# Kernel tuning notes

Hardware: AMD Instinct MI355X
Metric: run time of the kernel (lower is better)

Reference implementation:

```python
import jax, jax.numpy as jnp
import numpy as np

N_NODES = 50000
N_EDGES = 800000
IN_FEATS = 128
H_FEATS = 128
NUM_CLASSES = 64


def _linear_params(key, fan_in, fan_out):
    kw, kb = jax.random.split(key)
    bound = 1.0 / np.sqrt(fan_in)
    W = jax.random.uniform(kw, (fan_out, fan_in), minval=-bound, maxval=bound, dtype=jnp.float32)
    b = jax.random.uniform(kb, (fan_out,), minval=-bound, maxval=bound, dtype=jnp.float32)
    return W, b


def setup_inputs() -> dict:
    key = jax.random.key(0)
    k_feat, k_src, k_dst, k1, k2, k3 = jax.random.split(key, 6)
    in_feat = jax.random.normal(k_feat, (N_NODES, IN_FEATS), dtype=jnp.float32)
    src = jax.random.randint(k_src, (N_EDGES,), 0, N_NODES, dtype=jnp.int32)
    dst = jax.random.randint(k_dst, (N_EDGES,), 0, N_NODES, dtype=jnp.int32)
    W1, b1 = _linear_params(k1, IN_FEATS, H_FEATS)
    W2, b2 = _linear_params(k2, H_FEATS, H_FEATS)
    W3, b3 = _linear_params(k3, H_FEATS, NUM_CLASSES)
    return {"in_feat": in_feat, "W1": W1, "b1": b1, "W2": W2, "b2": b2,
            "W3": W3, "b3": b3, "src": src, "dst": dst}


def reference(in_feat, W1, b1, W2, b2, W3, b3, src, dst):
    N = in_feat.shape[0]

    def gin_layer(x, W, b):
        # DGL GINConv with eps=0: (x + sum of in-neighbor messages) -> Linear
        agg = jax.ops.segment_sum(x[src], dst, num_segments=N)  # [N, d]
        return jax.nn.relu((x + agg) @ W.T + b)

    h = gin_layer(in_feat, W1, b1)
    h = gin_layer(h, W2, b2)
    h = gin_layer(h, W3, b3)
    return h
```

## Files before the change

### kernel.cpp

```cpp
#include <hip/hip_runtime.h>

typedef _Float16 half8 __attribute__((ext_vector_type(8)));
typedef float floatx4 __attribute__((ext_vector_type(4)));
typedef unsigned int uintx4 __attribute__((ext_vector_type(4)));

union AB { uint4 u; half8 h; };
union H2 { unsigned int u; _Float16 h[2]; };
union US16 { uintx4 u[2]; unsigned short s[16]; };

#define CAPLOG 6
#define CAP 64

__global__ __launch_bounds__(256) void histA_init_k(
    const int* __restrict__ dst, int* __restrict__ histG, int E, int nbins,
    const float* __restrict__ F, const float* __restrict__ W1,
    const float* __restrict__ W2, const float* __restrict__ W3,
    _Float16* __restrict__ hX, _Float16* __restrict__ W1h,
    _Float16* __restrict__ W2h, _Float16* __restrict__ W3h,
    _Float16* __restrict__ hZ,
    int n4f, int n4w1, int n4w2, int n4w3, int zoffX4, int zoffZ4) {
    int t = threadIdx.x;
    if (blockIdx.x < 256) {
        __shared__ int h[256];
        h[t] = 0;
        __syncthreads();
        int per = (E + 255) / 256;
        int beg = blockIdx.x * per;
        int end = min(E, beg + per);
        for (int e = beg + t; e < end; e += 256)
            atomicAdd(&h[dst[e] >> 8], 1);
        __syncthreads();
        for (int i = t; i < nbins; i += 256)
            histG[i * 256 + blockIdx.x] = h[i];
        return;
    }
    int i = (blockIdx.x - 256) * 256 + t;
    const float* X;
    _Float16* O;
    int j;
    if (i < n4f) { X = F; O = hX; j = i; }
    else if (i < n4f + n4w1) { X = W1; O = W1h; j = i - n4f; }
    else if (i < n4f + n4w1 + n4w2) { X = W2; O = W2h; j = i - n4f - n4w1; }
    else if (i < n4f + n4w1 + n4w2 + n4w3) { X = W3; O = W3h; j = i - n4f - n4w1 - n4w2; }
    else {
        int z = i - (n4f + n4w1 + n4w2 + n4w3);
        if (z < 16) ((uint4*)hX)[zoffX4 + z] = make_uint4(0, 0, 0, 0);
        else if (z < 24) ((uint4*)hZ)[zoffZ4 + (z - 16)] = make_uint4(0, 0, 0, 0);
        return;
    }
    float4 v = reinterpret_cast<const float4*>(X)[j];
    union { uint2 u; _Float16 h[4]; } o;
    o.h[0] = (_Float16)v.x; o.h[1] = (_Float16)v.y;
    o.h[2] = (_Float16)v.z; o.h[3] = (_Float16)v.w;
    reinterpret_cast<uint2*>(O)[j] = o.u;
}

__global__ __launch_bounds__(1024) void scan1_k(const int* __restrict__ x,
                                                int* __restrict__ inc,
                                                int* __restrict__ partial, int n) {
    __shared__ int sd[1024];
    int t = threadIdx.x;
    int v = blockIdx.x * 1024 + t;
    sd[t] = (v < n) ? x[v] : 0;
    __syncthreads();
    for (int off = 1; off < 1024; off <<= 1) {
        int val = (t >= off) ? sd[t - off] : 0;
        __syncthreads();
        sd[t] += val;
        __syncthreads();
    }
    if (v < n) inc[v] = sd[t];
    if (t == 1023) partial[blockIdx.x] = sd[1023];
}

__global__ __launch_bounds__(256) void scatterB_k(const int* __restrict__ src,
                                                  const int* __restrict__ dst,
                                                  const int* __restrict__ inc,
                                                  const int* __restrict__ histG,
                                                  const int* __restrict__ partial, int nparts,
                                                  unsigned int* __restrict__ binned,
                                                  int E, int nbins) {
    __shared__ int cur[256];
    __shared__ int pp[64];
    int t = threadIdx.x, blk = blockIdx.x;
    if (t < 64) {
        int v = (t < nparts) ? partial[t] : 0;
        for (int off = 1; off < 64; off <<= 1) {
            int n = __shfl_up(v, off, 64);
            if (t >= off) v += n;
        }
        int ex = __shfl_up(v, 1, 64);
        if (t == 0) ex = 0;
        pp[t] = ex;
    }
    __syncthreads();
    for (int i = t; i < nbins; i += 256) {
        int idx = i * 256 + blk;
        cur[i] = inc[idx] + pp[idx >> 10] - histG[idx];
    }
    __syncthreads();
    int per = (E + 255) / 256;
    int beg = blk * per;
    int end = min(E, beg + per);
    for (int e = beg + t; e < end; e += 256) {
        int d = dst[e];
        int s = src[e];
        int pos = atomicAdd(&cur[d >> 8], 1);
        binned[pos] = ((unsigned int)(d & 255) << 16) | (unsigned int)s;
    }
}

__global__ __launch_bounds__(256) void binB_k(const unsigned int* __restrict__ binned,
                                              const int* __restrict__ inc,
                                              const int* __restrict__ histG,
                                              const int* __restrict__ partial, int nparts,
                                              unsigned short* __restrict__ col,
                                              int* __restrict__ cnt,
                                              int N, int E, int nbins) {
    __shared__ unsigned short lcol[256 * CAP];
    __shared__ int lcnt[256];
    __shared__ int pp[64];
    __shared__ int bounds[2];
    int t = threadIdx.x;
    int b = blockIdx.x;
    if (t < 64) {
        int v = (t < nparts) ? partial[t] : 0;
        for (int off = 1; off < 64; off <<= 1) {
            int n = __shfl_up(v, off, 64);
            if (t >= off) v += n;
        }
        int ex = __shfl_up(v, 1, 64);
        if (t == 0) ex = 0;
        pp[t] = ex;
    }
    unsigned int* lcol32 = (unsigned int*)lcol;
    for (int i = t; i < 256 * CAP / 2; i += 256) lcol32[i] = 0xFFFFFFFFu;
    lcnt[t] = 0;
    __syncthreads();
    if (t == 0) {
        int i0 = b * 256;
        bounds[0] = inc[i0] + pp[i0 >> 10] - histG[i0];
    } else if (t == 1) {
        if (b == nbins - 1) bounds[1] = E;
        else {
            int i1 = (b + 1) * 256;
            bounds[1] = inc[i1] + pp[i1 >> 10] - histG[i1];
        }
    }
    __syncthreads();
    int beg = bounds[0], end = bounds[1];
    for (int e = beg + t; e < end; e += 256) {
        unsigned int u = binned[e];
        int dl = u >> 16;
        int pos = atomicAdd(&lcnt[dl], 1);
        if (pos < CAP) lcol[(dl << CAPLOG) + pos] = (unsigned short)(u & 0xFFFFu);
    }
    __syncthreads();
    int base = b << 8;
    int nodes = min(256, N - base);
    uint4* colg = (uint4*)(col + ((size_t)base << CAPLOG));
    const uint4* coll = (const uint4*)lcol;
    for (int i = t; i < nodes * 8; i += 256) colg[i] = coll[i];
    for (int i = t; i < nodes; i += 256) cnt[base + i] = lcnt[i];
}

__global__ __launch_bounds__(256) void aggregate_k(const _Float16* __restrict__ X,
                                                   const int* __restrict__ cnt,
                                                   const unsigned short* __restrict__ col,
                                                   _Float16* __restrict__ Y,
                                                   int nnodes) {
    int b = blockIdx.x;
    int xcd = b & 7;
    int h = xcd >> 2;
    int ng = (b >> 3) * 4 + (xcd & 3);
    int lane = threadIdx.x & 63;
    int fl = lane & 31;
    int node = ng * 8 + (threadIdx.x >> 6) * 2 + (lane >> 5);
    if (node >= nnodes) return;
    const unsigned int* X32 = (const unsigned int*)X;
    int hoff = h << 5;

    int deg = cnt[node];
    if (deg > CAP) deg = CAP;
    int degp = (deg + 15) & ~15;
    const unsigned short* c = col + ((size_t)node << CAPLOG);

    float a[8], bb[8];
#pragma unroll
    for (int j = 0; j < 8; j++) { a[j] = 0.f; bb[j] = 0.f; }

    for (int e = 0; e < degp; e += 16) {
        US16 ix;
        ix.u[0] = *reinterpret_cast<const uintx4*>(c + e);
        ix.u[1] = *reinterpret_cast<const uintx4*>(c + e + 8);
        H2 u[16];
#pragma unroll
        for (int j = 0; j < 16; j++) {
            int s = (int)ix.s[j];
            s = (s < nnodes) ? s : nnodes;
            u[j].u = X32[(size_t)s * 64 + hoff + fl];
        }
#pragma unroll
        for (int j = 0; j < 8; j++) {
            a[j] += (float)u[j].h[0] + (float)u[j + 8].h[0];
            bb[j] += (float)u[j].h[1] + (float)u[j + 8].h[1];
        }
    }

    H2 xs, r;
    xs.u = X32[(size_t)node * 64 + hoff + fl];
    float s0 = ((a[0] + a[1]) + (a[2] + a[3])) + ((a[4] + a[5]) + (a[6] + a[7]));
    float s1 = ((bb[0] + bb[1]) + (bb[2] + bb[3])) + ((bb[4] + bb[5]) + (bb[6] + bb[7]));
    r.h[0] = (_Float16)((float)xs.h[0] + s0);
    r.h[1] = (_Float16)((float)xs.h[1] + s1);
    __builtin_nontemporal_store(r.u, reinterpret_cast<unsigned int*>(Y) + (size_t)node * 64 + hoff + fl);
}

__global__ __launch_bounds__(256) void agg_final_k(const _Float16* __restrict__ Z,
                                                   const int* __restrict__ cnt,
                                                   const unsigned short* __restrict__ col,
                                                   const float* __restrict__ bias,
                                                   float* __restrict__ out, int nnodes) {
    int lane = threadIdx.x & 63;
    int fl = lane & 31;
    int node = blockIdx.x * 8 + (threadIdx.x >> 6) * 2 + (lane >> 5);
    if (node >= nnodes) return;
    const unsigned int* Z32 = (const unsigned int*)Z;

    int deg = cnt[node];
    if (deg > CAP) deg = CAP;
    int degp = (deg + 15) & ~15;
    const unsigned short* c = col + ((size_t)node << CAPLOG);

    float a[8], bb[8];
#pragma unroll
    for (int j = 0; j < 8; j++) { a[j] = 0.f; bb[j] = 0.f; }

    for (int e = 0; e < degp; e += 16) {
        US16 ix;
        ix.u[0] = *reinterpret_cast<const uintx4*>(c + e);
        ix.u[1] = *reinterpret_cast<const uintx4*>(c + e + 8);
        H2 u[16];
#pragma unroll
        for (int j = 0; j < 16; j++) {
            int s = (int)ix.s[j];
            s = (s < nnodes) ? s : nnodes;
            u[j].u = Z32[(size_t)s * 32 + fl];
        }
#pragma unroll
        for (int j = 0; j < 8; j++) {
            a[j] += (float)u[j].h[0] + (float)u[j + 8].h[0];
            bb[j] += (float)u[j].h[1] + (float)u[j + 8].h[1];
        }
    }

    H2 xs;
    xs.u = Z32[(size_t)node * 32 + fl];
    float2 bv = reinterpret_cast<const float2*>(bias)[fl];
    float s0 = ((a[0] + a[1]) + (a[2] + a[3])) + ((a[4] + a[5]) + (a[6] + a[7]));
    float s1 = ((bb[0] + bb[1]) + (bb[2] + bb[3])) + ((bb[4] + bb[5]) + (bb[6] + bb[7]));
    float2 r;
    r.x = fmaxf((float)xs.h[0] + s0 + bv.x, 0.f);
    r.y = fmaxf((float)xs.h[1] + s1 + bv.y, 0.f);
    reinterpret_cast<float2*>(out)[(size_t)node * 32 + fl] = r;
}

template <int NOUT, bool RAW>
__global__ __launch_bounds__(256) void gemm_mfma_k(const _Float16* __restrict__ Y,
                                                   const _Float16* __restrict__ Wh,
                                                   const float* __restrict__ bias,
                                                   _Float16* __restrict__ out, int nnodes) {
    constexpr int NT = NOUT / 16;
    constexpr int WSTR = 136;
    __shared__ _Float16 Wl[NOUT * WSTR];
    __shared__ float Bl[NOUT];

    const int t = threadIdx.x;
    for (int p = t; p < NOUT * 16; p += 256) {
        int f = p >> 4;
        int kq = (p & 15) * 8;
        uint4 u = *reinterpret_cast<const uint4*>(Wh + f * 128 + kq);
        *reinterpret_cast<uint4*>(&Wl[f * WSTR + kq]) = u;
    }
    if (!RAW && t < NOUT) Bl[t] = bias[t];
    __syncthreads();

    const int wave = t >> 6;
    const int lane = t & 63;
    const int quad = lane >> 4;
    const int fcol = lane & 15;
    const int m_base = (blockIdx.x * 4 + wave) * 16;
    const int row = m_base + fcol;
    const bool rowok = row < nnodes;

    floatx4 acc[NT];
#pragma unroll
    for (int ft = 0; ft < NT; ft++) acc[ft] = (floatx4){0.f, 0.f, 0.f, 0.f};

    const uint4* Yrow = reinterpret_cast<const uint4*>(Y + (size_t)row * 128);
#pragma unroll
    for (int step = 0; step < 4; step++) {
        AB a;
        if (rowok) a.u = Yrow[step * 4 + quad];
        else       a.u = make_uint4(0u, 0u, 0u, 0u);
#pragma unroll
        for (int ft = 0; ft < NT; ft++) {
            half8 b = *reinterpret_cast<const half8*>(
                &Wl[(ft * 16 + fcol) * WSTR + step * 32 + quad * 8]);
            acc[ft] = __builtin_amdgcn_mfma_f32_16x16x32_f16(a.h, b, acc[ft], 0, 0, 0);
        }
    }

#pragma unroll
    for (int ft = 0; ft < NT; ft++) {
        int f = ft * 16 + fcol;
        float bv = RAW ? 0.f : Bl[f];
#pragma unroll
        for (int r = 0; r < 4; r++) {
            int node = m_base + quad * 4 + r;
            if (node < nnodes) {
                float v = acc[ft][r] + bv;
                if (!RAW) v = fmaxf(v, 0.f);
                out[(size_t)node * NOUT + f] = (_Float16)v;
            }
        }
    }
}

extern "C" void kernel_launch(void* const* d_in, const int* in_sizes, int n_in,
                              void* d_out, int out_size, void* d_ws, size_t ws_size,
                              hipStream_t stream) {
    const float* in_feat = (const float*)d_in[0];
    const float* W1 = (const float*)d_in[1];
    const float* b1 = (const float*)d_in[2];
    const float* W2 = (const float*)d_in[3];
    const float* b2 = (const float*)d_in[4];
    const float* W3 = (const float*)d_in[5];
    const float* b3 = (const float*)d_in[6];
    const int* src = (const int*)d_in[7];
    const int* dst = (const int*)d_in[8];
    float* out = (float*)d_out;

    const int N = in_sizes[0] / 128;
    const int E = in_sizes[7];
    const int szW1 = in_sizes[1];
    const int szW2 = in_sizes[3];
    const int szW3 = in_sizes[5];
    const int nbins = (N + 255) >> 8;
    const int nhist = nbins * 256;

    char* p = (char*)d_ws;
    int* cnt = (int*)p;               p += (size_t)N * 4;
    unsigned short* col = (unsigned short*)p; p += (size_t)N * CAP * 2;
    int* histG = (int*)p;             p += (size_t)nhist * 4;
    int* incS = (int*)p;              p += (size_t)nhist * 4;
    int* partial = (int*)p;           p += 256;
    unsigned int* binned = (unsigned int*)p; p += (size_t)E * 4;
    _Float16* hX = (_Float16*)p;      p += (size_t)(N + 1) * 128 * 2;
    _Float16* hB = (_Float16*)p;      p += (size_t)N * 128 * 2;
    _Float16* hZ = (_Float16*)p;      p += (size_t)(N + 1) * 64 * 2;
    _Float16* W1h = (_Float16*)p;     p += (size_t)szW1 * 2;
    _Float16* W2h = (_Float16*)p;     p += (size_t)szW2 * 2;
    _Float16* W3h = (_Float16*)p;     p += (size_t)szW3 * 2;

    const int nblk_scan = (nhist + 1023) / 1024;

    {
        int n4f = N * 128 / 4;
        int total = n4f + szW1 / 4 + szW2 / 4 + szW3 / 4 + 32;
        int iblk = (total + 255) / 256;
        histA_init_k<<<256 + iblk, 256, 0, stream>>>(dst, histG, E, nbins,
                                                     in_feat, W1, W2, W3,
                                                     hX, W1h, W2h, W3h, hZ,
                                                     n4f, szW1 / 4, szW2 / 4, szW3 / 4,
                                                     N * 16, N * 8);
    }
    scan1_k<<<nblk_scan, 1024, 0, stream>>>(histG, incS, partial, nhist);
    scatterB_k<<<256, 256, 0, stream>>>(src, dst, incS, histG, partial, nblk_scan,
                                        binned, E, nbins);
    binB_k<<<nbins, 256, 0, stream>>>(binned, incS, histG, partial, nblk_scan,
                                      col, cnt, N, E, nbins);

    const int ngrp8 = (N + 7) / 8;
    const int nblk_agg = ((ngrp8 + 3) / 4) * 8;
    const int nblk_gemm = (N + 63) / 64;
    aggregate_k<<<nblk_agg, 256, 0, stream>>>(hX, cnt, col, hB, N);
    gemm_mfma_k<128, false><<<nblk_gemm, 256, 0, stream>>>(hB, W1h, b1, hX, N);
    aggregate_k<<<nblk_agg, 256, 0, stream>>>(hX, cnt, col, hB, N);
    gemm_mfma_k<128, false><<<nblk_gemm, 256, 0, stream>>>(hB, W2h, b2, hX, N);
    gemm_mfma_k<64, true><<<nblk_gemm, 256, 0, stream>>>(hX, W3h, nullptr, hZ, N);
    agg_final_k<<<(N + 7) / 8, 256, 0, stream>>>(hZ, cnt, col, b3, out, N);
}
```

Measured before the change: 264.3 us.

## Use packed fp16 accumulation and one wave per node in aggregation

The aggregation kernels now accumulate neighbor features with packed half2 adds into 16 fp16 partial accumulators, converting to fp32 only for the final reduction, instead of converting every value to float. The main aggregate kernel also drops the XCD-aware split of feature halves across blocks and assigns one full 64-lane wave per node covering all 128 features. This cuts conversion and ALU work and simplifies indexing, but fp16 partial sums lose precision and the L2 locality of the previous XCD mapping is given up.

New measurement: 238.7 us. -9.7%, faster.

```diff
diff --git a/kernel.cpp b/kernel.cpp
--- a/kernel.cpp
+++ b/kernel.cpp
@@ -1,11 +1,13 @@
 #include <hip/hip_runtime.h>
 
 typedef _Float16 half8 __attribute__((ext_vector_type(8)));
+typedef _Float16 half2v __attribute__((ext_vector_type(2)));
 typedef float floatx4 __attribute__((ext_vector_type(4)));
 typedef unsigned int uintx4 __attribute__((ext_vector_type(4)));
 
 union AB { uint4 u; half8 h; };
 union H2 { unsigned int u; _Float16 h[2]; };
+union H2P { unsigned int u; half2v h; };
 union US16 { uintx4 u[2]; unsigned short s[16]; };
 
 #define CAPLOG 6
@@ -169,51 +171,45 @@
                                                    const unsigned short* __restrict__ col,
                                                    _Float16* __restrict__ Y,
                                                    int nnodes) {
-    int b = blockIdx.x;
-    int xcd = b & 7;
-    int h = xcd >> 2;
-    int ng = (b >> 3) * 4 + (xcd & 3);
+    int w = blockIdx.x * 4 + (threadIdx.x >> 6);
     int lane = threadIdx.x & 63;
-    int fl = lane & 31;
-    int node = ng * 8 + (threadIdx.x >> 6) * 2 + (lane >> 5);
-    if (node >= nnodes) return;
-    const unsigned int* X32 = (const unsigned int*)X;
-    int hoff = h << 5;
-
-    int deg = cnt[node];
+    if (w >= nnodes) return;
+    const unsigned int* X32 = reinterpret_cast<const unsigned int*>(X);
+    int deg = cnt[w];
     if (deg > CAP) deg = CAP;
     int degp = (deg + 15) & ~15;
-    const unsigned short* c = col + ((size_t)node << CAPLOG);
-
-    float a[8], bb[8];
-#pragma unroll
-    for (int j = 0; j < 8; j++) { a[j] = 0.f; bb[j] = 0.f; }
+    const unsigned short* c = col + ((size_t)w << CAPLOG);
+
+    H2P acc[16];
+#pragma unroll
+    for (int j = 0; j < 16; j++) acc[j].u = 0u;
 
     for (int e = 0; e < degp; e += 16) {
         US16 ix;
         ix.u[0] = *reinterpret_cast<const uintx4*>(c + e);
         ix.u[1] = *reinterpret_cast<const uintx4*>(c + e + 8);
-        H2 u[16];
+        H2P u[16];
 #pragma unroll
         for (int j = 0; j < 16; j++) {
             int s = (int)ix.s[j];
             s = (s < nnodes) ? s : nnodes;
-            u[j].u = X32[(size_t)s * 64 + hoff + fl];
-        }
-#pragma unroll
-        for (int j = 0; j < 8; j++) {
-            a[j] += (float)u[j].h[0] + (float)u[j + 8].h[0];
-            bb[j] += (float)u[j].h[1] + (float)u[j + 8].h[1];
-        }
-    }
-
+            u[j].u = X32[(size_t)s * 64 + lane];
+        }
+#pragma unroll
+        for (int j = 0; j < 16; j++) acc[j].h += u[j].h;
+    }
+
+    float s0 = 0.f, s1 = 0.f;
+#pragma unroll
+    for (int j = 0; j < 16; j++) {
+        s0 += (float)acc[j].h[0];
+        s1 += (float)acc[j].h[1];
+    }
     H2 xs, r;
-    xs.u = X32[(size_t)node * 64 + hoff + fl];
-    float s0 = ((a[0] + a[1]) + (a[2] + a[3])) + ((a[4] + a[5]) + (a[6] + a[7]));
-    float s1 = ((bb[0] + bb[1]) + (bb[2] + bb[3])) + ((bb[4] + bb[5]) + (bb[6] + bb[7]));
+    xs.u = X32[(size_t)w * 64 + lane];
     r.h[0] = (_Float16)((float)xs.h[0] + s0);
     r.h[1] = (_Float16)((float)xs.h[1] + s1);
-    __builtin_nontemporal_store(r.u, reinterpret_cast<unsigned int*>(Y) + (size_t)node * 64 + hoff + fl);
+    __builtin_nontemporal_store(r.u, reinterpret_cast<unsigned int*>(Y) + (size_t)w * 64 + lane);
 }
 
 __global__ __launch_bounds__(256) void agg_final_k(const _Float16* __restrict__ Z,
@@ -232,15 +228,15 @@
     int degp = (deg + 15) & ~15;
     const unsigned short* c = col + ((size_t)node << CAPLOG);
 
-    float a[8], bb[8];
-#pragma unroll
-    for (int j = 0; j < 8; j++) { a[j] = 0.f; bb[j] = 0.f; }
+    H2P acc[16];
+#pragma unroll
+    for (int j = 0; j < 16; j++) acc[j].u = 0u;
 
     for (int e = 0; e < degp; e += 16) {
         US16 ix;
         ix.u[0] = *reinterpret_cast<const uintx4*>(c + e);
         ix.u[1] = *reinterpret_cast<const uintx4*>(c + e + 8);
-        H2 u[16];
+        H2P u[16];
 #pragma unroll
         for (int j = 0; j < 16; j++) {
             int s = (int)ix.s[j];
@@ -248,17 +244,18 @@
             u[j].u = Z32[(size_t)s * 32 + fl];
         }
 #pragma unroll
-        for (int j = 0; j < 8; j++) {
-            a[j] += (float)u[j].h[0] + (float)u[j + 8].h[0];
-            bb[j] += (float)u[j].h[1] + (float)u[j + 8].h[1];
-        }
-    }
-
+        for (int j = 0; j < 16; j++) acc[j].h += u[j].h;
+    }
+
+    float s0 = 0.f, s1 = 0.f;
+#pragma unroll
+    for (int j = 0; j < 16; j++) {
+        s0 += (float)acc[j].h[0];
+        s1 += (float)acc[j].h[1];
+    }
     H2 xs;
     xs.u = Z32[(size_t)node * 32 + fl];
     float2 bv = reinterpret_cast<const float2*>(bias)[fl];
-    float s0 = ((a[0] + a[1]) + (a[2] + a[3])) + ((a[4] + a[5]) + (a[6] + a[7]));
-    float s1 = ((bb[0] + bb[1]) + (bb[2] + bb[3])) + ((bb[4] + bb[5]) + (bb[6] + bb[7]));
     float2 r;
     r.x = fmaxf((float)xs.h[0] + s0 + bv.x, 0.f);
     r.y = fmaxf((float)xs.h[1] + s1 + bv.y, 0.f);
@@ -381,8 +378,7 @@
     binB_k<<<nbins, 256, 0, stream>>>(binned, incS, histG, partial, nblk_scan,
                                       col, cnt, N, E, nbins);
 
-    const int ngrp8 = (N + 7) / 8;
-    const int nblk_agg = ((ngrp8 + 3) / 4) * 8;
+    const int nblk_agg = (N + 3) / 4;
     const int nblk_gemm = (N + 63) / 64;
     aggregate_k<<<nblk_agg, 256, 0, stream>>>(hX, cnt, col, hB, N);
     gemm_mfma_k<128, false><<<nblk_gemm, 256, 0, stream>>>(hB, W1h, b1, hX, N);
```
